# Performance work log

Hardware: AMD Instinct MI355X
Metric: run time of the kernel (lower is better)

## Reference

```python
import jax, jax.numpy as jnp
import numpy as np
import math

B, T, D = 8, 512, 512
H_HEADS, DQ, DV = 8, 64, 64
N_LAYERS, D_HID = 6, 2048
VOCAB, N_CLASSES = 32000, 5
LN_EPS = 1e-5


def setup_inputs() -> dict:
    key = jax.random.key(0)
    ks = jax.random.split(key, 20)
    s = 0.02
    x = jax.random.randint(ks[0], (B, T), 0, VOCAB - 1)
    emb = jax.random.normal(ks[1], (VOCAB, D), jnp.float32) * s
    emb = emb.at[VOCAB - 1].set(0.0)  # padding_idx row is zero
    # per-layer params stacked on leading N axis; weights stored [in, out]
    Wq = jax.random.normal(ks[2], (N_LAYERS, D, H_HEADS * DQ), jnp.float32) * s
    bq = jnp.zeros((N_LAYERS, H_HEADS * DQ), jnp.float32)
    Wk = jax.random.normal(ks[3], (N_LAYERS, D, H_HEADS * DQ), jnp.float32) * s
    bk = jnp.zeros((N_LAYERS, H_HEADS * DQ), jnp.float32)
    Wv = jax.random.normal(ks[4], (N_LAYERS, D, H_HEADS * DV), jnp.float32) * s
    bv = jnp.zeros((N_LAYERS, H_HEADS * DV), jnp.float32)
    Wo = jax.random.normal(ks[5], (N_LAYERS, H_HEADS * DV, D), jnp.float32) * s
    bo = jnp.zeros((N_LAYERS, D), jnp.float32)
    gamma = jnp.ones((N_LAYERS, D), jnp.float32)
    beta = jnp.zeros((N_LAYERS, D), jnp.float32)
    W1 = jax.random.normal(ks[6], (N_LAYERS, D, D_HID), jnp.float32) * s
    b1 = jnp.zeros((N_LAYERS, D_HID), jnp.float32)
    W2 = jax.random.normal(ks[7], (N_LAYERS, D_HID, D), jnp.float32) * s
    b2 = jnp.zeros((N_LAYERS, D), jnp.float32)
    Wout = jax.random.normal(ks[8], (D * T, N_CLASSES), jnp.float32) * s
    bout = jnp.zeros((N_CLASSES,), jnp.float32)
    return dict(x=x, stage=0, emb=emb, Wq=Wq, bq=bq, Wk=Wk, bk=bk, Wv=Wv, bv=bv,
                Wo=Wo, bo=bo, gamma=gamma, beta=beta, W1=W1, b1=b1, W2=W2, b2=b2,
                Wout=Wout, bout=bout)


def _sinusoidal_pe(t, d):
    pos = jnp.arange(t, dtype=jnp.float32)[:, None]              # [T,1]
    inv = jnp.exp(jnp.arange(0, d, 2, dtype=jnp.float32) * (-math.log(10000.0) / d))
    ang = pos * inv[None, :]                                     # [T, D/2]
    pe = jnp.ones((t, d), jnp.float32)
    pe = pe.at[:, 0::2].set(jnp.sin(ang)).at[:, 1::2].set(jnp.cos(ang))
    return pe


def _layer_norm(x, g, b):
    mu = jnp.mean(x, -1, keepdims=True)
    var = jnp.mean((x - mu) ** 2, -1, keepdims=True)
    return g * (x - mu) * jax.lax.rsqrt(var + LN_EPS) + b


def _attn(x, wq, bq_, wk, bk_, wv, bv_, wo, bo_):
    b, t, _ = x.shape
    q = (x @ wq + bq_).reshape(b, t, H_HEADS, DQ).transpose(0, 2, 1, 3)  # [B,h,T,dq]
    k = (x @ wk + bk_).reshape(b, t, H_HEADS, DQ).transpose(0, 2, 1, 3)
    v = (x @ wv + bv_).reshape(b, t, H_HEADS, DV).transpose(0, 2, 1, 3)
    score = jnp.einsum('bhtd,bhsd->bhts', q, k)  # NOTE: no 1/sqrt(d) scaling, per source
    a = jax.nn.softmax(score, axis=-1)
    o = jnp.einsum('bhts,bhsv->bhtv', a, v)
    o = o.transpose(0, 2, 1, 3).reshape(b, t, H_HEADS * DV)
    return o @ wo + bo_


def reference(x, stage, emb, Wq, bq, Wk, bk, Wv, bv, Wo, bo, gamma, beta, W1, b1, W2, b2, Wout, bout):
    h = emb[x]                                   # [B,T,D]
    h = h + _sinusoidal_pe(h.shape[1], h.shape[2])[None]
    for i in range(N_LAYERS):
        res = h
        a = _attn(h, Wq[i], bq[i], Wk[i], bk[i], Wv[i], bv[i], Wo[i], bo[i])
        h = _layer_norm(a + res, gamma[i], beta[i])
        res = h
        f = jax.nn.relu(h @ W1[i] + b1[i]) @ W2[i] + b2[i]
        h = _layer_norm(f + res, gamma[i], beta[i])  # same LN params reused, per source
    out = h.reshape(h.shape[0], -1) @ Wout + bout
    return out
```

## Files before the change

### kernel.cpp

```cpp
#include <hip/hip_runtime.h>
#include <hip/hip_bf16.h>


typedef _Float16 f16_t;
typedef _Float16 f16x8 __attribute__((ext_vector_type(8)));
typedef _Float16 f16x4 __attribute__((ext_vector_type(4)));
typedef _Float16 f16x2 __attribute__((ext_vector_type(2)));
typedef float    f32x4 __attribute__((ext_vector_type(4)));

#define LSTR 3145728LL

__device__ __forceinline__ void gl_lds16(const f16_t* g, f16_t* l) {
    __builtin_amdgcn_global_load_lds(
        (const __attribute__((address_space(1))) unsigned int*)g,
        (__attribute__((address_space(3))) unsigned int*)l, 16, 0, 0);
}

template<int BM, int BN, int BK, int WR, int WC, int OUTF16, int RELU, int VOUT>
__global__ void __launch_bounds__(256)
gemm_kernel(const f16_t* __restrict__ A, const f16_t* __restrict__ B,
            const float* __restrict__ bias, void* __restrict__ Cout,
            f16_t* __restrict__ vt,
            int M, int N, int K, int lda, int ldb, int ldc, int zmod,
            long long sAhi, long long sAlo, long long sBhi, long long sBlo,
            long long sChi, long long sClo)
{
    constexpr int WMT = BM / WR;
    constexpr int WNT = BN / WC;
    constexpr int MR  = WMT / 16;
    constexpr int NR  = WNT / 16;
    constexpr int KK  = BK / 32;
    constexpr int CPR = BK / 8;
    constexpr int RS  = (BK == 32) ? 1 : 0;
    constexpr int IA  = BM * BK / 2048;
    constexpr int IB  = BN * BK / 2048;
    __shared__ __align__(16) f16_t As[2][BM][BK];
    __shared__ __align__(16) f16_t Bs[2][BN][BK];

    const int tid  = threadIdx.x;
    const int wid  = tid >> 6, lane = tid & 63;
    const int wr   = wid / WC, wc = wid % WC;
    const int z    = blockIdx.z;
    const int zh   = z / zmod, zl = z % zmod;
    const f16_t* Ab = A + (long long)zh * sAhi + (long long)zl * sAlo;
    const f16_t* Bb = B + (long long)zh * sBhi + (long long)zl * sBlo;
    const int m0 = blockIdx.x * BM;
    const int n0 = blockIdx.y * BN;

    f32x4 acc[MR][NR] = {};

    const f16_t* srcA[IA]; const f16_t* srcB[IB];
#pragma unroll
    for (int i = 0; i < IA; ++i) {
        const int c = i * 256 + tid, row = c / CPR;
        const int kch = (c % CPR) ^ ((row >> RS) & (CPR - 1));
        srcA[i] = Ab + (long long)(m0 + row) * lda + kch * 8;
    }
#pragma unroll
    for (int i = 0; i < IB; ++i) {
        const int c = i * 256 + tid, row = c / CPR;
        const int kch = (c % CPR) ^ ((row >> RS) & (CPR - 1));
        srcB[i] = Bb + (long long)(n0 + row) * ldb + kch * 8;
    }
    auto stage = [&](int bf_, int t) {
        const int k0 = t * BK;
#pragma unroll
        for (int i = 0; i < IA; ++i)
            gl_lds16(srcA[i] + k0, &As[bf_][0][0] + (i * 256 + wid * 64) * 8);
#pragma unroll
        for (int i = 0; i < IB; ++i)
            gl_lds16(srcB[i] + k0, &Bs[bf_][0][0] + (i * 256 + wid * 64) * 8);
    };

    const int l15 = lane & 15;
    const int g   = lane >> 4;
    int aoff[MR][KK], boff[NR][KK];
#pragma unroll
    for (int m = 0; m < MR; ++m) {
        const int row = wr * WMT + m * 16 + l15;
        const int swz = ((row >> RS) & (CPR - 1)) << 4;
#pragma unroll
        for (int kk = 0; kk < KK; ++kk)
            aoff[m][kk] = ((row * BK + kk * 32 + g * 8) * 2) ^ swz;
    }
#pragma unroll
    for (int n = 0; n < NR; ++n) {
        const int row = wc * WNT + n * 16 + l15;
        const int swz = ((row >> RS) & (CPR - 1)) << 4;
#pragma unroll
        for (int kk = 0; kk < KK; ++kk)
            boff[n][kk] = ((row * BK + kk * 32 + g * 8) * 2) ^ swz;
    }

    const int NT = K / BK;
    stage(0, 0);
    __syncthreads();

    int buf = 0;
    for (int t = 0; t < NT; ++t) {
        if (t + 1 < NT) stage(buf ^ 1, t + 1);
        const char* Al = (const char*)&As[buf][0][0];
        const char* Bl = (const char*)&Bs[buf][0][0];
        f16x8 af[MR][KK], bfr[NR][KK];
#pragma unroll
        for (int m = 0; m < MR; ++m)
#pragma unroll
            for (int kk = 0; kk < KK; ++kk) af[m][kk] = *(const f16x8*)(Al + aoff[m][kk]);
#pragma unroll
        for (int n = 0; n < NR; ++n)
#pragma unroll
            for (int kk = 0; kk < KK; ++kk) bfr[n][kk] = *(const f16x8*)(Bl + boff[n][kk]);
#pragma unroll
        for (int kk = 0; kk < KK; ++kk)
#pragma unroll
            for (int m = 0; m < MR; ++m)
#pragma unroll
                for (int n = 0; n < NR; ++n)
                    acc[m][n] = __builtin_amdgcn_mfma_f32_16x16x32_f16(af[m][kk], bfr[n][kk], acc[m][n], 0, 0, 0);
        __syncthreads();
        buf ^= 1;
    }

    const long long cOff = (long long)zh * sChi + (long long)zl * sClo;
    const int rbase = (lane >> 4) * 4;
#pragma unroll
    for (int m = 0; m < MR; ++m) {
        const int row = m0 + wr * WMT + m * 16 + rbase;
#pragma unroll
        for (int n = 0; n < NR; ++n) {
            const int col = n0 + wc * WNT + n * 16 + l15;
            const float bb = bias ? bias[col] : 0.0f;
            if (VOUT && col >= 1024) {
                const int hh = (col - 1024) >> 6, dv = (col - 1024) & 63;
                const int bb_ = row >> 9, t0 = row & 511;
                f16x4 v4;
#pragma unroll
                for (int r = 0; r < 4; ++r) v4[r] = (f16_t)(acc[m][n][r] + bb);
                *(f16x4*)&vt[((long long)((bb_ * 8 + hh) * 64 + dv)) * 512 + t0] = v4;
            } else {
#pragma unroll
                for (int r = 0; r < 4; ++r) {
                    float v = acc[m][n][r] + bb;
                    if (RELU) v = fmaxf(v, 0.0f);
                    const long long idx = cOff + (long long)(row + r) * ldc + col;
                    if (OUTF16) ((f16_t*)Cout)[idx] = (f16_t)v;
                    else        ((float*)Cout)[idx] = v;
                }
            }
        }
    }
}

__global__ void __launch_bounds__(256)
attn_flash_kernel(const f16_t* __restrict__ qkv, const f16_t* __restrict__ Vt,
                  f16_t* __restrict__ ao)
{
    __shared__ __align__(16) f16_t Ks[512 * 64];
    __shared__ __align__(16) f16_t Qs[64 * 64];
    __shared__ __align__(16) f16_t Ps[4][16 * 64];
    const int tid = threadIdx.x, wid = tid >> 6, lane = tid & 63;
    const int l15 = lane & 15, g = lane >> 4;
    const int z = blockIdx.y, b = z >> 3, hh = z & 7;
    const int q0 = blockIdx.x * 64;
    const f16_t* Kbase = qkv + (long long)b * 512 * 1536 + 512 + hh * 64;
    const f16_t* Qbase = qkv + (long long)(b * 512 + q0) * 1536 + hh * 64;
    const f16_t* Vbase = Vt + (long long)z * 32768;

#pragma unroll
    for (int i = 0; i < 16; ++i) {
        const int c = i * 256 + tid, t = c >> 3, j = c & 7;
        gl_lds16(Kbase + (long long)t * 1536 + ((j ^ (t & 7)) << 3), Ks + c * 8);
    }
#pragma unroll
    for (int i = 0; i < 2; ++i) {
        const int c = i * 256 + tid, t = c >> 3, j = c & 7;
        gl_lds16(Qbase + (long long)t * 1536 + ((j ^ (t & 7)) << 3), Qs + c * 8);
    }
    __syncthreads();

    const int q = wid * 16 + l15;
    f16x8 qf[2];
#pragma unroll
    for (int k = 0; k < 2; ++k)
        qf[k] = *(const f16x8*)(Qs + q * 64 + (((k * 4 + g) ^ (l15 & 7)) << 3));

    f32x4 ov[4] = {};
    float m_run = -1e30f, l_run = 0.0f;
    f16_t* Pw = &Ps[wid][0];

    for (int ck = 0; ck < 8; ++ck) {
        const int kc0 = ck * 64;
        f16x8 vf[4][2];
#pragma unroll
        for (int n = 0; n < 4; ++n)
#pragma unroll
            for (int k = 0; k < 2; ++k)
                vf[n][k] = *(const f16x8*)(Vbase + (n * 16 + l15) * 512 + kc0 + k * 32 + g * 8);
        f32x4 s[4] = {};
#pragma unroll
        for (int k = 0; k < 2; ++k)
#pragma unroll
            for (int m = 0; m < 4; ++m) {
                const int key = kc0 + m * 16 + l15;
                const f16x8 a = *(const f16x8*)(Ks + key * 64 + (((k * 4 + g) ^ (key & 7)) << 3));
                s[m] = __builtin_amdgcn_mfma_f32_16x16x32_f16(a, qf[k], s[m], 0, 0, 0);
            }
        float cmax = -1e30f;
#pragma unroll
        for (int m = 0; m < 4; ++m)
#pragma unroll
            for (int r = 0; r < 4; ++r) cmax = fmaxf(cmax, s[m][r]);
        cmax = fmaxf(cmax, __shfl_xor(cmax, 16, 64));
        cmax = fmaxf(cmax, __shfl_xor(cmax, 32, 64));
        const float mnew = fmaxf(m_run, cmax);
        const float corr = __expf(m_run - mnew);
        float csum = 0.0f;
#pragma unroll
        for (int m = 0; m < 4; ++m) {
            f16x4 p4;
#pragma unroll
            for (int r = 0; r < 4; ++r) {
                const float pe = __expf(s[m][r] - mnew);
                csum += pe;
                p4[r] = (f16_t)pe;
            }
            *(f16x4*)(Pw + l15 * 64 + ((((m * 2 + (g >> 1)) ^ (l15 & 7))) << 3) + ((g & 1) << 2)) = p4;
        }
        csum += __shfl_xor(csum, 16, 64);
        csum += __shfl_xor(csum, 32, 64);
        l_run = l_run * corr + csum;
        m_run = mnew;
        float cr[4];
#pragma unroll
        for (int r = 0; r < 4; ++r) cr[r] = __shfl(corr, g * 4 + r, 64);
#pragma unroll
        for (int n = 0; n < 4; ++n)
#pragma unroll
            for (int r = 0; r < 4; ++r) ov[n][r] *= cr[r];
#pragma unroll
        for (int k = 0; k < 2; ++k) {
            const f16x8 pf = *(const f16x8*)(Pw + l15 * 64 + (((k * 4 + g) ^ (l15 & 7)) << 3));
#pragma unroll
            for (int n = 0; n < 4; ++n)
                ov[n] = __builtin_amdgcn_mfma_f32_16x16x32_f16(pf, vf[n][k], ov[n], 0, 0, 0);
        }
    }

    const float inv = 1.0f / l_run;
    float ir[4];
#pragma unroll
    for (int r = 0; r < 4; ++r) ir[r] = __shfl(inv, g * 4 + r, 64);
#pragma unroll
    for (int n = 0; n < 4; ++n)
#pragma unroll
        for (int r = 0; r < 4; ++r) {
            const long long row = b * 512 + q0 + wid * 16 + g * 4 + r;
            ao[row * 512 + hh * 64 + n * 16 + l15] = (f16_t)(ov[n][r] * ir[r]);
        }
}

__global__ void wconv_kernel(const float* __restrict__ Wq, const float* __restrict__ Wk,
                             const float* __restrict__ Wv, const float* __restrict__ Wo,
                             const float* __restrict__ W1, const float* __restrict__ W2,
                             f16_t* __restrict__ wT)
{
    __shared__ float tile[32][33];
    const int t     = blockIdx.x;
    const int layer = t / 3072;
    const int r     = t % 3072;
    const float* src; f16_t* dst; int R, C, tt;
    if (r < 1024) {
        const int mat = r >> 8; tt = r & 255; R = 512; C = 512;
        const float* s4 = (mat == 0) ? Wq : (mat == 1) ? Wk : (mat == 2) ? Wv : Wo;
        src = s4 + (long long)layer * 262144;
        dst = wT + (long long)layer * LSTR + (long long)mat * 262144;
    } else if (r < 2048) {
        tt = r - 1024; R = 512; C = 2048;
        src = W1 + (long long)layer * 1048576;
        dst = wT + (long long)layer * LSTR + 1048576;
    } else {
        tt = r - 2048; R = 2048; C = 512;
        src = W2 + (long long)layer * 1048576;
        dst = wT + (long long)layer * LSTR + 2097152;
    }
    const int tC = C >> 5;
    const int tr = tt / tC, tc = tt % tC;
    const int r0 = tr * 32, c0 = tc * 32;
    const int tx = threadIdx.x, ty = threadIdx.y;
#pragma unroll
    for (int i = 0; i < 4; ++i)
        tile[ty + 8 * i][tx] = src[(long long)(r0 + ty + 8 * i) * C + c0 + tx];
    __syncthreads();
#pragma unroll
    for (int i = 0; i < 4; ++i)
        dst[(long long)(c0 + ty + 8 * i) * R + r0 + tx] = (f16_t)tile[tx][ty + 8 * i];
}

__global__ void biascat_kernel(const float* __restrict__ bq, const float* __restrict__ bk,
                               const float* __restrict__ bv, float* __restrict__ qkvb)
{
    const int i = blockIdx.x * 256 + threadIdx.x;
    if (i >= 9216) return;
    const int l = i / 1536, c = i % 1536;
    float v;
    if (c < 512)       v = bq[l * 512 + c];
    else if (c < 1024) v = bk[l * 512 + c - 512];
    else               v = bv[l * 512 + c - 1024];
    qkvb[i] = v;
}

__global__ void embed_kernel(const int* __restrict__ xt, const float* __restrict__ emb,
                             f16_t* __restrict__ hb)
{
    const int row = blockIdx.x;
    const int t   = row & 511;
    const int tok = xt[row];
    const int tid = threadIdx.x;
#pragma unroll
    for (int s = 0; s < 2; ++s) {
        const int d = tid + s * 256;
        const int i = d >> 1;
        const float inv = expf((float)(2 * i) * (-9.210340371976184f / 512.0f));
        const float ang = (float)t * inv;
        const float pe  = (d & 1) ? cosf(ang) : sinf(ang);
        hb[(long long)row * 512 + d] = (f16_t)(emb[(long long)tok * 512 + d] + pe);
    }
}

__global__ void __launch_bounds__(256)
add_ln_kernel(const f16_t* __restrict__ X, int ns, long long sstr,
              const float* __restrict__ bias,
              const float* __restrict__ g, const float* __restrict__ b,
              f16_t* __restrict__ Hf)
{
    const int wid = threadIdx.x >> 6, lane = threadIdx.x & 63;
    const long long row = (long long)blockIdx.x * 4 + wid;
    f16_t* h = Hf + row * 512;
    const int c0 = lane * 8;
    const f16x8 hv = *(const f16x8*)&h[c0];
    float v[8];
#pragma unroll
    for (int e = 0; e < 8; ++e) v[e] = (float)hv[e] + bias[c0 + e];
    for (int s = 0; s < ns; ++s) {
        const f16x8 xv = *(const f16x8*)&X[s * sstr + row * 512 + c0];
#pragma unroll
        for (int e = 0; e < 8; ++e) v[e] += (float)xv[e];
    }
    float sum = 0.0f, sq = 0.0f;
#pragma unroll
    for (int e = 0; e < 8; ++e) { sum += v[e]; sq += v[e] * v[e]; }
#pragma unroll
    for (int o = 1; o < 64; o <<= 1) {
        sum += __shfl_xor(sum, o, 64);
        sq  += __shfl_xor(sq,  o, 64);
    }
    const float mu = sum * (1.0f / 512.0f);
    float var = sq * (1.0f / 512.0f) - mu * mu;
    var = fmaxf(var, 0.0f);
    const float rs = rsqrtf(var + 1e-5f);
    f16x8 o8;
#pragma unroll
    for (int e = 0; e < 8; ++e)
        o8[e] = (f16_t)(g[c0 + e] * (v[e] - mu) * rs + b[c0 + e]);
    *(f16x8*)&h[c0] = o8;
}

__global__ void head_partial_kernel(const f16_t* __restrict__ hb, const float* __restrict__ Wout,
                                    float* __restrict__ partials)
{
    const int blk = blockIdx.x;
    const int b = blk >> 6, chunk = blk & 63;
    const int tid = threadIdx.x;
    const f16_t* hp = hb + (long long)b * 262144 + (long long)chunk * 4096;
    float a0 = 0, a1 = 0, a2 = 0, a3 = 0, a4 = 0;
    for (int it = 0; it < 16; ++it) {
        const int idx = it * 256 + tid;
        const float hv = (float)hp[idx];
        const float* w = Wout + ((long long)chunk * 4096 + idx) * 5;
        a0 += hv * w[0]; a1 += hv * w[1]; a2 += hv * w[2]; a3 += hv * w[3]; a4 += hv * w[4];
    }
#pragma unroll
    for (int o = 32; o > 0; o >>= 1) {
        a0 += __shfl_down(a0, o, 64); a1 += __shfl_down(a1, o, 64); a2 += __shfl_down(a2, o, 64);
        a3 += __shfl_down(a3, o, 64); a4 += __shfl_down(a4, o, 64);
    }
    __shared__ float sm[4][5];
    const int lane = tid & 63, w = tid >> 6;
    if (lane == 0) { sm[w][0] = a0; sm[w][1] = a1; sm[w][2] = a2; sm[w][3] = a3; sm[w][4] = a4; }
    __syncthreads();
    if (tid < 5)
        partials[(long long)blk * 5 + tid] = sm[0][tid] + sm[1][tid] + sm[2][tid] + sm[3][tid];
}

__global__ void head_final_kernel(const float* __restrict__ partials, const float* __restrict__ bout,
                                  float* __restrict__ out)
{
    const int tid = threadIdx.x;
    if (tid >= 40) return;
    const int b = tid / 5, c = tid % 5;
    float s = bout[c];
    const float* p = partials + (long long)b * 64 * 5 + c;
    for (int ck = 0; ck < 64; ++ck) s += p[ck * 5];
    out[tid] = s;
}

extern "C" void kernel_launch(void* const* d_in, const int* in_sizes, int n_in,
                              void* d_out, int out_size, void* d_ws, size_t ws_size,
                              hipStream_t stream)
{
    (void)in_sizes; (void)n_in; (void)out_size; (void)ws_size;
    const int*   x_tok = (const int*)  d_in[0];
    const float* emb   = (const float*)d_in[2];
    const float* Wq    = (const float*)d_in[3];
    const float* bq    = (const float*)d_in[4];
    const float* Wk    = (const float*)d_in[5];
    const float* bk    = (const float*)d_in[6];
    const float* Wv    = (const float*)d_in[7];
    const float* bv    = (const float*)d_in[8];
    const float* Wo    = (const float*)d_in[9];
    const float* bo    = (const float*)d_in[10];
    const float* gma   = (const float*)d_in[11];
    const float* bta   = (const float*)d_in[12];
    const float* W1    = (const float*)d_in[13];
    const float* b1    = (const float*)d_in[14];
    const float* W2    = (const float*)d_in[15];
    const float* b2    = (const float*)d_in[16];
    const float* Wout  = (const float*)d_in[17];
    const float* bout  = (const float*)d_in[18];

    char* ws = (char*)d_ws;
    size_t off = 0;
    auto take = [&](size_t bytes) { char* p = ws + off; off += (bytes + 255) & ~(size_t)255; return p; };
    f16_t* wT    = (f16_t*)take(18874368ULL * 2);
    f16_t* hb    = (f16_t*)take(2097152ULL * 2);
    f16_t* qkv   = (f16_t*)take(6291456ULL * 2);
    f16_t* Vt    = (f16_t*)take(2097152ULL * 2);
    f16_t* ao    = (f16_t*)take(2097152ULL * 2);
    f16_t* f1    = (f16_t*)take(8388608ULL * 2);
    f16_t* t16   = (f16_t*)take(4ULL * 2097152ULL * 2);
    float* qkvb  = (float*)take(9216ULL * 4);
    float* parts = (float*)take(2560ULL * 4);

    wconv_kernel <<<dim3(18432), dim3(32, 8), 0, stream>>>(Wq, Wk, Wv, Wo, W1, W2, wT);
    biascat_kernel<<<dim3(36), 256, 0, stream>>>(bq, bk, bv, qkvb);
    embed_kernel <<<dim3(4096), 256, 0, stream>>>(x_tok, emb, hb);

    for (int l = 0; l < 6; ++l) {
        const f16_t* wl = wT + (long long)l * LSTR;
        gemm_kernel<64,128,64,2,2,1,0,1><<<dim3(64,12,1),256,0,stream>>>(hb, wl, qkvb + l*1536,
            qkv, Vt, 4096,1536,512, 512,512,1536, 1, 0,0,0,0,0,0);
        attn_flash_kernel<<<dim3(8,64),256,0,stream>>>(qkv, Vt, ao);
        gemm_kernel<64,128,64,2,2,1,0,0><<<dim3(64,4,2),256,0,stream>>>(ao, wl + 786432, nullptr,
            t16, nullptr, 4096,512,256, 512,512,512, 1, 256LL,0LL, 256LL,0LL, 2097152LL,0LL);
        add_ln_kernel<<<dim3(1024),256,0,stream>>>(t16, 2, 2097152LL, bo + l*512,
            gma + l*512, bta + l*512, hb);
        gemm_kernel<128,128,32,2,2,1,1,0><<<dim3(32,16,1),256,0,stream>>>(hb, wl + 1048576, b1 + l*2048,
            f1, nullptr, 4096,2048,512, 512,512,2048, 1, 0,0,0,0,0,0);
        gemm_kernel<128,128,32,2,2,1,0,0><<<dim3(32,4,4),256,0,stream>>>(f1, wl + 2097152, nullptr,
            t16, nullptr, 4096,512,512, 2048,2048,512, 1, 512LL,0LL, 512LL,0LL, 2097152LL,0LL);
        add_ln_kernel<<<dim3(1024),256,0,stream>>>(t16, 4, 2097152LL, b2 + l*512,
            gma + l*512, bta + l*512, hb);
    }

    head_partial_kernel<<<dim3(512),256,0,stream>>>(hb, Wout, parts);
    head_final_kernel  <<<dim3(1),64,0,stream>>>(parts, bout, (float*)d_out);
}
```

Measured before the change: 566.1 us.

## Drop LDS staging in attention, merge setup kernels, fuse head reduction

The attention kernel no longer stages K and Q through shared memory. It loads K and Q fragments directly from global memory per chunk and raises wave priority around the MFMA blocks. The three setup kernels (weight transpose, embedding, bias concat) become one launch, and the head's two kernels become one that uses an atomic ticket so the last block does the final reduction. This cuts launch count and LDS use, which may raise occupancy, but attention now re-reads K from global/L2 in every block without coalesced staging.

Result: slower. 650.3 us (+14.9%).

```diff
diff --git a/kernel.cpp b/kernel.cpp
--- a/kernel.cpp
+++ b/kernel.cpp
@@ -155,8 +155,6 @@
 attn_flash_kernel(const f16_t* __restrict__ qkv, const f16_t* __restrict__ Vt,
                   f16_t* __restrict__ ao)
 {
-    __shared__ __align__(16) f16_t Ks[512 * 64];
-    __shared__ __align__(16) f16_t Qs[64 * 64];
     __shared__ __align__(16) f16_t Ps[4][16 * 64];
     const int tid = threadIdx.x, wid = tid >> 6, lane = tid & 63;
     const int l15 = lane & 15, g = lane >> 4;
@@ -166,23 +164,11 @@
     const f16_t* Qbase = qkv + (long long)(b * 512 + q0) * 1536 + hh * 64;
     const f16_t* Vbase = Vt + (long long)z * 32768;
 
-#pragma unroll
-    for (int i = 0; i < 16; ++i) {
-        const int c = i * 256 + tid, t = c >> 3, j = c & 7;
-        gl_lds16(Kbase + (long long)t * 1536 + ((j ^ (t & 7)) << 3), Ks + c * 8);
-    }
-#pragma unroll
-    for (int i = 0; i < 2; ++i) {
-        const int c = i * 256 + tid, t = c >> 3, j = c & 7;
-        gl_lds16(Qbase + (long long)t * 1536 + ((j ^ (t & 7)) << 3), Qs + c * 8);
-    }
-    __syncthreads();
-
     const int q = wid * 16 + l15;
     f16x8 qf[2];
 #pragma unroll
     for (int k = 0; k < 2; ++k)
-        qf[k] = *(const f16x8*)(Qs + q * 64 + (((k * 4 + g) ^ (l15 & 7)) << 3));
+        qf[k] = *(const f16x8*)(Qbase + (long long)q * 1536 + k * 32 + g * 8);
 
     f32x4 ov[4] = {};
     float m_run = -1e30f, l_run = 0.0f;
@@ -196,15 +182,22 @@
 #pragma unroll
             for (int k = 0; k < 2; ++k)
                 vf[n][k] = *(const f16x8*)(Vbase + (n * 16 + l15) * 512 + kc0 + k * 32 + g * 8);
+        f16x8 kf[4][2];
+#pragma unroll
+        for (int m = 0; m < 4; ++m) {
+            const int key = kc0 + m * 16 + l15;
+#pragma unroll
+            for (int k = 0; k < 2; ++k)
+                kf[m][k] = *(const f16x8*)(Kbase + (long long)key * 1536 + k * 32 + g * 8);
+        }
         f32x4 s[4] = {};
+        __builtin_amdgcn_s_setprio(1);
 #pragma unroll
         for (int k = 0; k < 2; ++k)
 #pragma unroll
-            for (int m = 0; m < 4; ++m) {
-                const int key = kc0 + m * 16 + l15;
-                const f16x8 a = *(const f16x8*)(Ks + key * 64 + (((k * 4 + g) ^ (key & 7)) << 3));
-                s[m] = __builtin_amdgcn_mfma_f32_16x16x32_f16(a, qf[k], s[m], 0, 0, 0);
-            }
+            for (int m = 0; m < 4; ++m)
+                s[m] = __builtin_amdgcn_mfma_f32_16x16x32_f16(kf[m][k], qf[k], s[m], 0, 0, 0);
+        __builtin_amdgcn_s_setprio(0);
         float cmax = -1e30f;
 #pragma unroll
         for (int m = 0; m < 4; ++m)
@@ -240,9 +233,11 @@
 #pragma unroll
         for (int k = 0; k < 2; ++k) {
             const f16x8 pf = *(const f16x8*)(Pw + l15 * 64 + (((k * 4 + g) ^ (l15 & 7)) << 3));
+            __builtin_amdgcn_s_setprio(1);
 #pragma unroll
             for (int n = 0; n < 4; ++n)
                 ov[n] = __builtin_amdgcn_mfma_f32_16x16x32_f16(pf, vf[n][k], ov[n], 0, 0, 0);
+            __builtin_amdgcn_s_setprio(0);
         }
     }
 
@@ -259,71 +254,73 @@
         }
 }
 
-__global__ void wconv_kernel(const float* __restrict__ Wq, const float* __restrict__ Wk,
-                             const float* __restrict__ Wv, const float* __restrict__ Wo,
-                             const float* __restrict__ W1, const float* __restrict__ W2,
-                             f16_t* __restrict__ wT)
+__global__ void __launch_bounds__(256)
+setup_kernel(const float* __restrict__ Wq, const float* __restrict__ Wk,
+             const float* __restrict__ Wv, const float* __restrict__ Wo,
+             const float* __restrict__ W1, const float* __restrict__ W2,
+             f16_t* __restrict__ wT,
+             const int* __restrict__ xt, const float* __restrict__ emb,
+             f16_t* __restrict__ hb,
+             const float* __restrict__ bq, const float* __restrict__ bk,
+             const float* __restrict__ bv, float* __restrict__ qkvb,
+             int* __restrict__ cnt)
 {
     __shared__ float tile[32][33];
-    const int t     = blockIdx.x;
-    const int layer = t / 3072;
-    const int r     = t % 3072;
-    const float* src; f16_t* dst; int R, C, tt;
-    if (r < 1024) {
-        const int mat = r >> 8; tt = r & 255; R = 512; C = 512;
-        const float* s4 = (mat == 0) ? Wq : (mat == 1) ? Wk : (mat == 2) ? Wv : Wo;
-        src = s4 + (long long)layer * 262144;
-        dst = wT + (long long)layer * LSTR + (long long)mat * 262144;
-    } else if (r < 2048) {
-        tt = r - 1024; R = 512; C = 2048;
-        src = W1 + (long long)layer * 1048576;
-        dst = wT + (long long)layer * LSTR + 1048576;
+    const int blk = blockIdx.x;
+    const int tid = threadIdx.x;
+    if (blk < 18432) {
+        const int layer = blk / 3072;
+        const int r     = blk % 3072;
+        const float* src; f16_t* dst; int R, C, tt;
+        if (r < 1024) {
+            const int mat = r >> 8; tt = r & 255; R = 512; C = 512;
+            const float* s4 = (mat == 0) ? Wq : (mat == 1) ? Wk : (mat == 2) ? Wv : Wo;
+            src = s4 + (long long)layer * 262144;
+            dst = wT + (long long)layer * LSTR + (long long)mat * 262144;
+        } else if (r < 2048) {
+            tt = r - 1024; R = 512; C = 2048;
+            src = W1 + (long long)layer * 1048576;
+            dst = wT + (long long)layer * LSTR + 1048576;
+        } else {
+            tt = r - 2048; R = 2048; C = 512;
+            src = W2 + (long long)layer * 1048576;
+            dst = wT + (long long)layer * LSTR + 2097152;
+        }
+        const int tC = C >> 5;
+        const int tr = tt / tC, tc = tt % tC;
+        const int r0 = tr * 32, c0 = tc * 32;
+        const int tx = tid & 31, ty = tid >> 5;
+#pragma unroll
+        for (int i = 0; i < 4; ++i)
+            tile[ty + 8 * i][tx] = src[(long long)(r0 + ty + 8 * i) * C + c0 + tx];
+        __syncthreads();
+#pragma unroll
+        for (int i = 0; i < 4; ++i)
+            dst[(long long)(c0 + ty + 8 * i) * R + r0 + tx] = (f16_t)tile[tx][ty + 8 * i];
+    } else if (blk < 18432 + 4096) {
+        const int row = blk - 18432;
+        const int t   = row & 511;
+        const int tok = xt[row];
+#pragma unroll
+        for (int s = 0; s < 2; ++s) {
+            const int d = tid + s * 256;
+            const int i = d >> 1;
+            const float inv = expf((float)(2 * i) * (-9.210340371976184f / 512.0f));
+            const float ang = (float)t * inv;
+            const float pe  = (d & 1) ? cosf(ang) : sinf(ang);
+            hb[(long long)row * 512 + d] = (f16_t)(emb[(long long)tok * 512 + d] + pe);
+        }
     } else {
-        tt = r - 2048; R = 2048; C = 512;
-        src = W2 + (long long)layer * 1048576;
-        dst = wT + (long long)layer * LSTR + 2097152;
-    }
-    const int tC = C >> 5;
-    const int tr = tt / tC, tc = tt % tC;
-    const int r0 = tr * 32, c0 = tc * 32;
-    const int tx = threadIdx.x, ty = threadIdx.y;
-#pragma unroll
-    for (int i = 0; i < 4; ++i)
-        tile[ty + 8 * i][tx] = src[(long long)(r0 + ty + 8 * i) * C + c0 + tx];
-    __syncthreads();
-#pragma unroll
-    for (int i = 0; i < 4; ++i)
-        dst[(long long)(c0 + ty + 8 * i) * R + r0 + tx] = (f16_t)tile[tx][ty + 8 * i];
-}
-
-__global__ void biascat_kernel(const float* __restrict__ bq, const float* __restrict__ bk,
-                               const float* __restrict__ bv, float* __restrict__ qkvb)
-{
-    const int i = blockIdx.x * 256 + threadIdx.x;
-    if (i >= 9216) return;
-    const int l = i / 1536, c = i % 1536;
-    float v;
-    if (c < 512)       v = bq[l * 512 + c];
-    else if (c < 1024) v = bk[l * 512 + c - 512];
-    else               v = bv[l * 512 + c - 1024];
-    qkvb[i] = v;
-}
-
-__global__ void embed_kernel(const int* __restrict__ xt, const float* __restrict__ emb,
-                             f16_t* __restrict__ hb)
-{
-    const int row = blockIdx.x;
-    const int t   = row & 511;
-    const int tok = xt[row];
-    const int tid = threadIdx.x;
-#pragma unroll
-    for (int s = 0; s < 2; ++s) {
-        const int d = tid + s * 256;
-        const int i = d >> 1;
-        const float inv = expf((float)(2 * i) * (-9.210340371976184f / 512.0f));
-        const float ang = (float)t * inv;
-        const float pe  = (d & 1) ? cosf(ang) : sinf(ang);
-        hb[(long long)row * 512 + d] = (f16_t)(emb[(long long)tok * 512 + d] + pe);
+        const int i = (blk - 22528) * 256 + tid;
+        if (i < 9216) {
+            const int l = i / 1536, c = i % 1536;
+            float v;
+            if (c < 512)       v = bq[l * 512 + c];
+            else if (c < 1024) v = bk[l * 512 + c - 512];
+            else               v = bv[l * 512 + c - 1024];
+            qkvb[i] = v;
+        }
+        if (blk == 22528 && tid == 0) *cnt = 0;
     }
 }
 
@@ -365,8 +362,10 @@
     *(f16x8*)&h[c0] = o8;
 }
 
-__global__ void head_partial_kernel(const f16_t* __restrict__ hb, const float* __restrict__ Wout,
-                                    float* __restrict__ partials)
+__global__ void __launch_bounds__(256)
+head_kernel(const f16_t* __restrict__ hb, const float* __restrict__ Wout,
+            const float* __restrict__ bout, float* __restrict__ partials,
+            int* __restrict__ cnt, float* __restrict__ out)
 {
     const int blk = blockIdx.x;
     const int b = blk >> 6, chunk = blk & 63;
@@ -385,23 +384,26 @@
         a3 += __shfl_down(a3, o, 64); a4 += __shfl_down(a4, o, 64);
     }
     __shared__ float sm[4][5];
+    __shared__ int ticket;
     const int lane = tid & 63, w = tid >> 6;
     if (lane == 0) { sm[w][0] = a0; sm[w][1] = a1; sm[w][2] = a2; sm[w][3] = a3; sm[w][4] = a4; }
     __syncthreads();
     if (tid < 5)
         partials[(long long)blk * 5 + tid] = sm[0][tid] + sm[1][tid] + sm[2][tid] + sm[3][tid];
-}
-
-__global__ void head_final_kernel(const float* __restrict__ partials, const float* __restrict__ bout,
-                                  float* __restrict__ out)
-{
-    const int tid = threadIdx.x;
-    if (tid >= 40) return;
-    const int b = tid / 5, c = tid % 5;
-    float s = bout[c];
-    const float* p = partials + (long long)b * 64 * 5 + c;
-    for (int ck = 0; ck < 64; ++ck) s += p[ck * 5];
-    out[tid] = s;
+    __threadfence();
+    __syncthreads();
+    if (tid == 0) ticket = atomicAdd(cnt, 1);
+    __syncthreads();
+    if (ticket == 511) {
+        __threadfence();
+        if (tid < 40) {
+            const int bb = tid / 5, c = tid % 5;
+            float s = bout[c];
+            const float* p = partials + (long long)bb * 64 * 5 + c;
+            for (int ck = 0; ck < 64; ++ck) s += p[ck * 5];
+            out[tid] = s;
+        }
+    }
 }
 
 extern "C" void kernel_launch(void* const* d_in, const int* in_sizes, int n_in,
@@ -440,10 +442,10 @@
     f16_t* t16   = (f16_t*)take(4ULL * 2097152ULL * 2);
     float* qkvb  = (float*)take(9216ULL * 4);
     float* parts = (float*)take(2560ULL * 4);
-
-    wconv_kernel <<<dim3(18432), dim3(32, 8), 0, stream>>>(Wq, Wk, Wv, Wo, W1, W2, wT);
-    biascat_kernel<<<dim3(36), 256, 0, stream>>>(bq, bk, bv, qkvb);
-    embed_kernel <<<dim3(4096), 256, 0, stream>>>(x_tok, emb, hb);
+    int*   cnt   = (int*)  take(256);
+
+    setup_kernel<<<dim3(22564), 256, 0, stream>>>(Wq, Wk, Wv, Wo, W1, W2, wT,
+                                                  x_tok, emb, hb, bq, bk, bv, qkvb, cnt);
 
     for (int l = 0; l < 6; ++l) {
         const f16_t* wl = wT + (long long)l * LSTR;
@@ -462,6 +464,5 @@
             gma + l*512, bta + l*512, hb);
     }
 
-    head_partial_kernel<<<dim3(512),256,0,stream>>>(hb, Wout, parts);
-    head_final_kernel  <<<dim3(1),64,0,stream>>>(parts, bout, (float*)d_out);
-}
+    head_kernel<<<dim3(512),256,0,stream>>>(hb, Wout, bout, parts, cnt, (float*)d_out);
+}
```
